# Kernel optimization log

Measured on AMD Instinct MI355X. Metric: run time of the kernel, lower is better.

## Reference

```python
import jax, jax.numpy as jnp
import numpy as np

LATENT_CH = 64  # feature_ch // 8


def conv1x1(x, w):
    # Conv2dLayer with kernel_size=1, bias=False, activation='linear':
    # weight_gain = 1/sqrt(in_channels * 1)
    gain = 1.0 / np.sqrt(w.shape[1])
    return jnp.einsum('bchw,oc->bohw', x, w * gain)


def casual_attention(q, k, v):
    # q,k,v: [B, C, N] / [B, C, M]; score = q^T k, softmax over keys, out = score @ v^T
    score = jnp.einsum('bcn,bcm->bnm', q, k)
    score = jax.nn.softmax(score, axis=-1)
    return jnp.einsum('bnm,bcm->bnc', score, v)  # [B, N, C]


def reference(feature_map, concepts, w_theta, w_phi, w_g, w_o, gamma_sa, gamma_moca):
    B, C, H, W = feature_map.shape
    L = LATENT_CH
    HW = H * W

    # ---- SelfAttention ----
    th = conv1x1(feature_map, w_theta).reshape(B, L, HW)
    ph = conv1x1(feature_map, w_phi).reshape(B, L, HW)
    g = conv1x1(feature_map, w_g).reshape(B, L, HW)
    # torch does .view(-1, L, H, W) on a [B, HW, L] tensor -> raw memory reinterpret
    lat = casual_attention(th, ph, g).reshape(B, L, H, W)
    sa_out = gamma_sa * conv1x1(lat, w_o) + feature_map

    # ---- MomentumConceptAttention (theta and o shared with SA, trainable_conv=False) ----
    enc = conv1x1(sa_out, w_theta).reshape(B, L, HW)
    phi_c = concepts.T[None]                      # [1, L, P]  (torch.no_grad on concepts)
    phi_c = jnp.broadcast_to(phi_c, (B, L, concepts.shape[0]))
    lat2 = casual_attention(enc, phi_c, phi_c).reshape(B, L, H, W)
    out = gamma_moca * conv1x1(lat2, w_o) + sa_out
    return out


def setup_inputs() -> dict:
    key = jax.random.key(0)
    ks = jax.random.split(key, 8)
    B, C, H, W = 8, 512, 64, 64
    L, P = LATENT_CH, 256
    return {
        'feature_map': jax.random.normal(ks[0], (B, C, H, W), jnp.float32),
        'concepts': jax.random.normal(ks[1], (P, L), jnp.float32),
        'w_theta': jax.random.normal(ks[2], (L, C), jnp.float32),
        'w_phi': jax.random.normal(ks[3], (L, C), jnp.float32),
        'w_g': jax.random.normal(ks[4], (L, C), jnp.float32),
        'w_o': jax.random.normal(ks[5], (C, L), jnp.float32),
        'gamma_sa': jnp.float32(0.1),
        'gamma_moca': jnp.float32(0.1),
    }
```

## Files before the change

kernel.cpp:

```cpp
#include <hip/hip_runtime.h>
#include <math.h>

#define HW   4096
#define CINP 512
#define LCH  64

typedef short bf8 __attribute__((ext_vector_type(8)));
typedef float f4  __attribute__((ext_vector_type(4)));

__device__ __forceinline__ unsigned short f2bf(float x) {
    union { float f; unsigned int u; } v; v.f = x;
    return (unsigned short)((v.u + 0x7fffu + ((v.u >> 16) & 1u)) >> 16);
}
__device__ __forceinline__ bf8 ldbf8(const unsigned short* p) {
    uint4 u = *(const uint4*)p;
    return __builtin_bit_cast(bf8, u);
}
__device__ __forceinline__ unsigned int cvtpk(float a, float b) {
    unsigned int r;
    asm volatile("v_cvt_pk_bf16_f32 %0, %1, %2" : "=v"(r) : "v"(a), "v"(b));
    return r;
}

__global__ __launch_bounds__(256) void precast(
    const float* __restrict__ wt, const float* __restrict__ wp,
    const float* __restrict__ wg, const float* __restrict__ wo,
    const float* __restrict__ conc,
    unsigned short* __restrict__ WB, unsigned short* __restrict__ WO,
    unsigned short* __restrict__ CK, unsigned short* __restrict__ CV)
{
    const float gain = 0.04419417382415922f;
    int id = blockIdx.x * 256 + threadIdx.x;
    if (id < 98304) {
        int o = id >> 9, k = id & 511;
        const float* w = (o < 64) ? wt : (o < 128) ? wp : wg;
        WB[id] = f2bf(w[(o & 63) * 512 + k] * gain);
    } else if (id < 131072) {
        int j = id - 98304;
        WO[j] = f2bf(wo[j]);
    } else if (id < 147456) {
        int j = id - 131072;
        CK[j] = f2bf(conc[j]);
    } else if (id < 163840) {
        int j = id - 147456;
        int l = j >> 8, m = j & 255;
        CV[j] = f2bf(conc[m * 64 + l]);
    }
}

__global__ __launch_bounds__(256) void cast_transpose(const float* __restrict__ x,
                                                      unsigned short* __restrict__ XT)
{
    __shared__ unsigned short Lb[64][72];
    const int t  = threadIdx.x;
    const int n0 = blockIdx.x * 64, c0 = blockIdx.y * 64, b = blockIdx.z;
    const float* xb = x + ((size_t)b * CINP + c0) * HW + n0;
    const int cc = t >> 4, n4 = (t & 15) * 4;
    #pragma unroll
    for (int i = 0; i < 4; i++) {
        int c = cc + i * 16;
        float4 v = *(const float4*)(xb + (size_t)c * HW + n4);
        Lb[n4 + 0][c] = f2bf(v.x);
        Lb[n4 + 1][c] = f2bf(v.y);
        Lb[n4 + 2][c] = f2bf(v.z);
        Lb[n4 + 3][c] = f2bf(v.w);
    }
    __syncthreads();
    const int n = t & 63, cb0 = t >> 6;
    unsigned short* orow = XT + ((size_t)b * HW + n0 + n) * CINP + c0;
    #pragma unroll
    for (int i = 0; i < 2; i++) {
        int cb = cb0 + i * 4;
        *(uint4*)(orow + cb * 8) = *(const uint4*)&Lb[n][cb * 8];
    }
}

__global__ __launch_bounds__(256) void lat_transpose(const unsigned short* __restrict__ A,
                                                     unsigned short* __restrict__ LT)
{
    __shared__ unsigned short Ls[64][72];
    const int t = threadIdx.x, s0 = blockIdx.x * 64, b = blockIdx.y;
    const unsigned short* ab = A + (size_t)b * LCH * HW;
    #pragma unroll
    for (int it = 0; it < 2; it++) {
        int c = (t >> 3) + it * 32, s8 = (t & 7) * 8;
        union { uint4 u; unsigned short s[8]; } v;
        v.u = *(const uint4*)(ab + (size_t)c * HW + s0 + s8);
        #pragma unroll
        for (int i = 0; i < 8; i++) Ls[s8 + i][c] = v.s[i];
    }
    __syncthreads();
    unsigned short* ob = LT + ((size_t)b * HW + s0) * LCH;
    #pragma unroll
    for (int it = 0; it < 2; it++) {
        int s = (t >> 3) + it * 32, c8 = (t & 7);
        *(uint4*)(ob + (size_t)s * LCH + c8 * 8) = *(const uint4*)&Ls[s][c8 * 8];
    }
}

template <int NRT>
__global__ __launch_bounds__(256) void qkv_gemm(unsigned short* XT,
                                                const unsigned short* __restrict__ WB,
                                                unsigned short* __restrict__ VL)
{
    const int t = threadIdx.x;
    const int wave = t >> 6, lane = t & 63, quad = lane >> 4, lidx = lane & 15;
    const int b = blockIdx.y;
    const int ncol = blockIdx.x * 64 + wave * 16 + lidx;
    unsigned short* xrow = XT + ((size_t)b * HW + ncol) * CINP;

    f4 acc[NRT];
    #pragma unroll
    for (int r = 0; r < NRT; r++) acc[r] = (f4){0.f, 0.f, 0.f, 0.f};

    for (int kk = 0; kk < 16; kk++) {
        const int k0 = kk * 32 + quad * 8;
        bf8 bq = ldbf8(xrow + k0);
        #pragma unroll
        for (int rt = 0; rt < NRT; rt++) {
            bf8 aw = ldbf8(WB + (size_t)(rt * 16 + lidx) * CINP + k0);
            acc[rt] = __builtin_amdgcn_mfma_f32_16x16x32_bf16(aw, bq, acc[rt], 0, 0, 0);
        }
    }

    #pragma unroll
    for (int rt = 0; rt < NRT; rt++) {
        if (rt < 8) {
            union { unsigned short s[4]; uint2 u; } pk;
            #pragma unroll
            for (int r = 0; r < 4; r++) pk.s[r] = f2bf(acc[rt][r]);
            int off = (rt < 4) ? (rt * 16 + quad * 4) : (64 + (rt - 4) * 16 + quad * 4);
            *(uint2*)(xrow + off) = pk.u;
        } else {
            #pragma unroll
            for (int r = 0; r < 4; r++) {
                int l = (rt - 8) * 16 + quad * 4 + r;
                VL[((size_t)b * LCH + l) * HW + ncol] = f2bf(acc[rt][r]);
            }
        }
    }
}

__global__ __launch_bounds__(512) void flash(
    const unsigned short* Qb, size_t qbat,
    const unsigned short* Kb, size_t krow, size_t kbat,
    const unsigned short* Vb, size_t vrow, size_t vbat,
    unsigned short* __restrict__ Aout, int nkeys)
{
    __shared__ __align__(16) unsigned short Ks[2][32][72];
    __shared__ __align__(16) unsigned short Vs[2][64][40];
    __shared__ __align__(16) unsigned short Ps[8][16][40];

    const int t = threadIdx.x;
    const int wave = t >> 6, lane = t & 63, quad = lane >> 4, lidx = lane & 15;
    const int b = blockIdx.y, q0 = blockIdx.x * 128 + wave * 16;

    const unsigned short* qp = Qb + (size_t)b * qbat;
    const unsigned short* kp = Kb + (size_t)b * kbat;
    const unsigned short* vp = Vb + (size_t)b * vbat;

    const bool stK = t < 256;
    const int krt = t >> 3, kch = (t & 7) * 8;
    const int u = t & 255, vrt = u >> 2, vch = (u & 3) * 8;

    bf8 qa[2];
    #pragma unroll
    for (int kh = 0; kh < 2; kh++)
        qa[kh] = ldbf8(qp + (size_t)(q0 + lidx) * CINP + kh * 32 + quad * 8);

    f4 O[4];
    float Lp = 0.f;
    #pragma unroll
    for (int lt = 0; lt < 4; lt++) O[lt] = (f4){0.f, 0.f, 0.f, 0.f};

    const int nt = nkeys >> 5;

    if (stK) *(uint4*)&Ks[0][krt][kch] = *(const uint4*)(kp + (size_t)krt * krow + kch);
    else     *(uint4*)&Vs[0][vrt][vch] = *(const uint4*)(vp + (size_t)vrt * vrow + vch);
    __syncthreads();

    for (int tl = 0; tl < nt; tl++) {
        const int cur = tl & 1;
        const bool pf = (tl + 1 < nt);
        uint4 pre;
        if (pf) {
            const int m1 = (tl + 1) * 32;
            pre = stK ? *(const uint4*)(kp + (size_t)(m1 + krt) * krow + kch)
                      : *(const uint4*)(vp + (size_t)vrt * vrow + m1 + vch);
        }

        bf8 kf[2][2];
        #pragma unroll
        for (int ms = 0; ms < 2; ms++)
            #pragma unroll
            for (int kh = 0; kh < 2; kh++)
                kf[ms][kh] = *(const bf8*)&Ks[cur][ms * 16 + lidx][kh * 32 + quad * 8];

        f4 S[2];
        #pragma unroll
        for (int ms = 0; ms < 2; ms++) {
            f4 s = (f4){0.f, 0.f, 0.f, 0.f};
            s = __builtin_amdgcn_mfma_f32_16x16x32_bf16(kf[ms][0], qa[0], s, 0, 0, 0);
            s = __builtin_amdgcn_mfma_f32_16x16x32_bf16(kf[ms][1], qa[1], s, 0, 0, 0);
            S[ms] = s;
        }

        #pragma unroll
        for (int ms = 0; ms < 2; ms++) {
            float p0 = __expf(S[ms][0]);
            float p1 = __expf(S[ms][1]);
            float p2 = __expf(S[ms][2]);
            float p3 = __expf(S[ms][3]);
            Lp += (p0 + p1) + (p2 + p3);
            uint2 pk;
            pk.x = cvtpk(p0, p1);
            pk.y = cvtpk(p2, p3);
            *(uint2*)&Ps[wave][lidx][ms * 16 + quad * 4] = pk;
        }

        bf8 pfr = *(const bf8*)&Ps[wave][lidx][quad * 8];
        #pragma unroll
        for (int lt = 0; lt < 4; lt++) {
            bf8 vf = *(const bf8*)&Vs[cur][lt * 16 + lidx][quad * 8];
            O[lt] = __builtin_amdgcn_mfma_f32_16x16x32_bf16(pfr, vf, O[lt], 0, 0, 0);
        }

        if (pf) {
            if (stK) *(uint4*)&Ks[cur ^ 1][krt][kch] = pre;
            else     *(uint4*)&Vs[cur ^ 1][vrt][vch] = pre;
        }
        __syncthreads();
    }

    float s = Lp;
    s += __shfl_xor(s, 16);
    s += __shfl_xor(s, 32);
    const float inv = 1.f / s;
    #pragma unroll
    for (int r = 0; r < 4; r++) {
        float iv = __shfl(inv, quad * 4 + r);
        size_t n = (size_t)b * HW + q0 + quad * 4 + r;
        #pragma unroll
        for (int lt = 0; lt < 4; lt++)
            Aout[n * LCH + lt * 16 + lidx] = f2bf(O[lt][r] * iv);
    }
}

__global__ __launch_bounds__(256) void conv_o(const unsigned short* __restrict__ LT,
                                              const unsigned short* __restrict__ WO,
                                              const float* __restrict__ res,
                                              const float* __restrict__ gamma_p,
                                              float* __restrict__ out,
                                              unsigned short* ST)
{
    const int t = threadIdx.x;
    const int wave = t >> 6, lane = t & 63, quad = lane >> 4, lidx = lane & 15;
    const int b = blockIdx.z, o0 = blockIdx.y * 64;
    const int scol = blockIdx.x * 64 + wave * 16 + lidx;
    const unsigned short* arow = LT + ((size_t)b * HW + scol) * LCH;

    f4 acc[4];
    #pragma unroll
    for (int ot = 0; ot < 4; ot++) acc[ot] = (f4){0.f, 0.f, 0.f, 0.f};

    #pragma unroll
    for (int kh = 0; kh < 2; kh++) {
        bf8 bq = ldbf8(arow + kh * 32 + quad * 8);
        #pragma unroll
        for (int ot = 0; ot < 4; ot++) {
            bf8 af = ldbf8(WO + (size_t)(o0 + ot * 16 + lidx) * LCH + kh * 32 + quad * 8);
            acc[ot] = __builtin_amdgcn_mfma_f32_16x16x32_bf16(af, bq, acc[ot], 0, 0, 0);
        }
    }

    const float scale = gamma_p[0] * 0.125f;
    #pragma unroll
    for (int ot = 0; ot < 4; ot++) {
        float v[4];
        #pragma unroll
        for (int r = 0; r < 4; r++) {
            size_t idx = ((size_t)b * CINP + o0 + ot * 16 + quad * 4 + r) * HW + scol;
            v[r] = fmaf(scale, acc[ot][r], res[idx]);
            out[idx] = v[r];
        }
        if (ST) {
            union { unsigned short s[4]; uint2 u; } pk;
            #pragma unroll
            for (int r = 0; r < 4; r++) pk.s[r] = f2bf(v[r]);
            *(uint2*)(ST + ((size_t)b * HW + scol) * CINP + o0 + ot * 16 + quad * 4) = pk.u;
        }
    }
}

extern "C" void kernel_launch(void* const* d_in, const int* in_sizes, int n_in,
                              void* d_out, int out_size, void* d_ws, size_t ws_size,
                              hipStream_t stream)
{
    const float* f    = (const float*)d_in[0];
    const float* conc = (const float*)d_in[1];
    const float* wt   = (const float*)d_in[2];
    const float* wp   = (const float*)d_in[3];
    const float* wg   = (const float*)d_in[4];
    const float* wo   = (const float*)d_in[5];
    const float* gsa  = (const float*)d_in[6];
    const float* gmo  = (const float*)d_in[7];
    float* out = (float*)d_out;

    char* ws = (char*)d_ws;
    unsigned short* XT = (unsigned short*)ws;
    unsigned short* VL = (unsigned short*)(ws + ((size_t)32 << 20));
    unsigned short* LT = VL;
    unsigned short* A1 = (unsigned short*)(ws + ((size_t)36 << 20));
    unsigned short* WB = (unsigned short*)(ws + ((size_t)40 << 20));
    unsigned short* WO = WB + 192 * 512;
    unsigned short* CK = WO + 512 * 64;
    unsigned short* CV = CK + 256 * 64;

    dim3 blk256(256), blk512(512);

    precast<<<640, blk256, 0, stream>>>(wt, wp, wg, wo, conc, WB, WO, CK, CV);
    cast_transpose<<<dim3(64, 8, 8), blk256, 0, stream>>>(f, XT);

    qkv_gemm<12><<<dim3(64, 8), blk256, 0, stream>>>(XT, WB, VL);
    flash<<<dim3(32, 8), blk512, 0, stream>>>(
        XT, (size_t)HW * CINP,
        XT + 64, CINP, (size_t)HW * CINP,
        VL, HW, (size_t)LCH * HW,
        A1, HW);
    lat_transpose<<<dim3(64, 8), blk256, 0, stream>>>(A1, LT);
    conv_o<<<dim3(64, 8, 8), blk256, 0, stream>>>(LT, WO, f, gsa, out, XT );

    qkv_gemm<4><<<dim3(64, 8), blk256, 0, stream>>>(XT , WB , nullptr);
    flash<<<dim3(32, 8), blk512, 0, stream>>>(
        XT, (size_t)HW * CINP,
        CK, LCH, 0,
        CV, 256, 0,
        A1 , 256);
    lat_transpose<<<dim3(64, 8), blk256, 0, stream>>>(A1, LT);
    conv_o<<<dim3(64, 8, 8), blk256, 0, stream>>>(LT, WO, out, gmo, out, nullptr);
}
```

Measured before the change: 393.7 us.

## Double key tile size and pass P via permlane swaps instead of LDS

The flash attention kernel now processes 64 keys per iteration instead of 32, and every thread loads both a K and a V chunk, which halves the number of loop iterations and block barriers. The softmax probabilities are rearranged from the score MFMA output layout into the A-operand layout with permlane32/permlane16 swap intrinsics, removing the per-wave Ps shared buffer and its LDS round trip. The cost is more registers per thread and a larger shared-memory footprint for the doubled K/V buffers. The permute pattern must exactly match the MFMA operand layout to stay correct.

```diff
diff --git a/kernel.cpp b/kernel.cpp
--- a/kernel.cpp
+++ b/kernel.cpp
@@ -7,6 +7,7 @@
 
 typedef short bf8 __attribute__((ext_vector_type(8)));
 typedef float f4  __attribute__((ext_vector_type(4)));
+typedef unsigned int u32x2 __attribute__((ext_vector_type(2)));
 
 __device__ __forceinline__ unsigned short f2bf(float x) {
     union { float f; unsigned int u; } v; v.f = x;
@@ -147,9 +148,8 @@
     const unsigned short* Vb, size_t vrow, size_t vbat,
     unsigned short* __restrict__ Aout, int nkeys)
 {
-    __shared__ __align__(16) unsigned short Ks[2][32][72];
-    __shared__ __align__(16) unsigned short Vs[2][64][40];
-    __shared__ __align__(16) unsigned short Ps[8][16][40];
+    __shared__ __align__(16) unsigned short Ks[2][64][72];
+    __shared__ __align__(16) unsigned short Vs[2][2][64][40];
 
     const int t = threadIdx.x;
     const int wave = t >> 6, lane = t & 63, quad = lane >> 4, lidx = lane & 15;
@@ -159,9 +159,11 @@
     const unsigned short* kp = Kb + (size_t)b * kbat;
     const unsigned short* vp = Vb + (size_t)b * vbat;
 
-    const bool stK = t < 256;
-    const int krt = t >> 3, kch = (t & 7) * 8;
-    const int u = t & 255, vrt = u >> 2, vch = (u & 3) * 8;
+    const int srow = t >> 3, sch = t & 7;
+    const int vseg = sch >> 2, vcs = sch & 3;
+    const unsigned short* ksrc = kp + (size_t)srow * krow + sch * 8;
+    const unsigned short* vsrc = vp + (size_t)srow * vrow + sch * 8;
+    const size_t kstep = (size_t)64 * krow;
 
     bf8 qa[2];
     #pragma unroll
@@ -173,61 +175,68 @@
     #pragma unroll
     for (int lt = 0; lt < 4; lt++) O[lt] = (f4){0.f, 0.f, 0.f, 0.f};
 
-    const int nt = nkeys >> 5;
-
-    if (stK) *(uint4*)&Ks[0][krt][kch] = *(const uint4*)(kp + (size_t)krt * krow + kch);
-    else     *(uint4*)&Vs[0][vrt][vch] = *(const uint4*)(vp + (size_t)vrt * vrow + vch);
+    const int nt = nkeys >> 6;
+
+    *(uint4*)&Ks[0][srow][sch * 8]       = *(const uint4*)ksrc;
+    *(uint4*)&Vs[0][vseg][srow][vcs * 8] = *(const uint4*)vsrc;
+    ksrc += kstep; vsrc += 64;
     __syncthreads();
 
     for (int tl = 0; tl < nt; tl++) {
         const int cur = tl & 1;
-        const bool pf = (tl + 1 < nt);
-        uint4 pre;
-        if (pf) {
-            const int m1 = (tl + 1) * 32;
-            pre = stK ? *(const uint4*)(kp + (size_t)(m1 + krt) * krow + kch)
-                      : *(const uint4*)(vp + (size_t)vrt * vrow + m1 + vch);
-        }
-
-        bf8 kf[2][2];
-        #pragma unroll
-        for (int ms = 0; ms < 2; ms++)
+        const bool pfv = (tl + 1 < nt);
+        uint4 kq, vq;
+        if (pfv) {
+            kq = *(const uint4*)ksrc;
+            vq = *(const uint4*)vsrc;
+            ksrc += kstep; vsrc += 64;
+        }
+
+        bf8 kf[4][2];
+        #pragma unroll
+        for (int ms = 0; ms < 4; ms++)
             #pragma unroll
             for (int kh = 0; kh < 2; kh++)
                 kf[ms][kh] = *(const bf8*)&Ks[cur][ms * 16 + lidx][kh * 32 + quad * 8];
 
-        f4 S[2];
-        #pragma unroll
-        for (int ms = 0; ms < 2; ms++) {
+        f4 S[4];
+        #pragma unroll
+        for (int ms = 0; ms < 4; ms++) {
             f4 s = (f4){0.f, 0.f, 0.f, 0.f};
             s = __builtin_amdgcn_mfma_f32_16x16x32_bf16(kf[ms][0], qa[0], s, 0, 0, 0);
             s = __builtin_amdgcn_mfma_f32_16x16x32_bf16(kf[ms][1], qa[1], s, 0, 0, 0);
             S[ms] = s;
         }
 
-        #pragma unroll
-        for (int ms = 0; ms < 2; ms++) {
-            float p0 = __expf(S[ms][0]);
-            float p1 = __expf(S[ms][1]);
-            float p2 = __expf(S[ms][2]);
-            float p3 = __expf(S[ms][3]);
-            Lp += (p0 + p1) + (p2 + p3);
-            uint2 pk;
-            pk.x = cvtpk(p0, p1);
-            pk.y = cvtpk(p2, p3);
-            *(uint2*)&Ps[wave][lidx][ms * 16 + quad * 4] = pk;
-        }
-
-        bf8 pfr = *(const bf8*)&Ps[wave][lidx][quad * 8];
-        #pragma unroll
-        for (int lt = 0; lt < 4; lt++) {
-            bf8 vf = *(const bf8*)&Vs[cur][lt * 16 + lidx][quad * 8];
-            O[lt] = __builtin_amdgcn_mfma_f32_16x16x32_bf16(pfr, vf, O[lt], 0, 0, 0);
-        }
-
-        if (pf) {
-            if (stK) *(uint4*)&Ks[cur ^ 1][krt][kch] = pre;
-            else     *(uint4*)&Vs[cur ^ 1][vrt][vch] = pre;
+        bf8 pa[2];
+        #pragma unroll
+        for (int p = 0; p < 2; p++) {
+            float e00 = __expf(S[2 * p][0]),     e01 = __expf(S[2 * p][1]);
+            float e02 = __expf(S[2 * p][2]),     e03 = __expf(S[2 * p][3]);
+            float e10 = __expf(S[2 * p + 1][0]), e11 = __expf(S[2 * p + 1][1]);
+            float e12 = __expf(S[2 * p + 1][2]), e13 = __expf(S[2 * p + 1][3]);
+            Lp += ((e00 + e01) + (e02 + e03)) + ((e10 + e11) + (e12 + e13));
+            unsigned int A = cvtpk(e00, e01), B = cvtpk(e02, e03);
+            unsigned int C = cvtpk(e10, e11), D = cvtpk(e12, e13);
+            u32x2 ac = __builtin_amdgcn_permlane32_swap(A, C, false, false);
+            u32x2 xz = __builtin_amdgcn_permlane16_swap(ac.x, ac.y, false, false);
+            u32x2 bd = __builtin_amdgcn_permlane32_swap(B, D, false, false);
+            u32x2 yw = __builtin_amdgcn_permlane16_swap(bd.x, bd.y, false, false);
+            uint4 pu; pu.x = xz.x; pu.y = yw.x; pu.z = xz.y; pu.w = yw.y;
+            pa[p] = __builtin_bit_cast(bf8, pu);
+        }
+
+        #pragma unroll
+        for (int g = 0; g < 2; g++)
+            #pragma unroll
+            for (int lt = 0; lt < 4; lt++) {
+                bf8 vf = *(const bf8*)&Vs[cur][g][lt * 16 + lidx][quad * 8];
+                O[lt] = __builtin_amdgcn_mfma_f32_16x16x32_bf16(pa[g], vf, O[lt], 0, 0, 0);
+            }
+
+        if (pfv) {
+            *(uint4*)&Ks[cur ^ 1][srow][sch * 8]       = kq;
+            *(uint4*)&Vs[cur ^ 1][vseg][srow][vcs * 8] = vq;
         }
         __syncthreads();
     }
```

Result: faster. 363.0 us (-7.8%).
